# Kernel tuning notes

Measured on AMD Instinct MI355X. Metric: run time of the kernel, lower is better.

The kernel has to match this reference:

```python
import jax, jax.numpy as jnp
import numpy as np

B, S, D = 8, 4096, 64
NEG = 10000.0


def setup_inputs() -> dict:
    key = jax.random.key(0)
    k1, k2, k3, k4 = jax.random.split(key, 4)
    query = jax.random.normal(k1, (B, S, D), dtype=jnp.float32)
    k_ = jax.random.normal(k2, (B, S, D), dtype=jnp.float32)
    v_ = jax.random.normal(k3, (B, S, D), dtype=jnp.float32)
    # padding mask [B, Sk]: mostly valid, tail padded for some rows
    lens = jax.random.randint(k4, (B,), S // 2, S + 1)
    mask = jnp.arange(S)[None, :] < lens[:, None]
    return {"query": query, "key": k_, "value": v_, "mask": mask}


def reference(query, key, value, mask):
    d = query.shape[-1]
    scale = 1.0 / jnp.sqrt(jnp.asarray(d, dtype=query.dtype))
    # e: [B, Sq, Sk]
    e = jnp.einsum("bqd,bkd->bqk", query, key) * scale
    # causal (history_only) mask: key index > query index gets -10000
    q_idx = jnp.arange(query.shape[1])[:, None]
    k_idx = jnp.arange(key.shape[1])[None, :]
    e = e - NEG * (k_idx > q_idx).astype(e.dtype)[None, :, :]
    # padding mask [B, 1, Sk]
    e = e - NEG * (1.0 - mask.astype(e.dtype))[:, None, :]
    attention = jax.nn.softmax(e, axis=-1)
    return jnp.einsum("bqk,bkd->bqd", attention, value)
```

## Files before the change

### kernel.cpp

```cpp
#include <hip/hip_runtime.h>
#include <hip/hip_bf16.h>

#define B_N 8
#define S_N 4096
#define D_N 64
#define NQT 64
#define TILE_BYTES 8192
#define SLOT_BYTES 8704

typedef __attribute__((ext_vector_type(8))) short bf16x8;
typedef __attribute__((ext_vector_type(4))) float f32x4;
typedef __attribute__((ext_vector_type(16))) float f32x16;
typedef unsigned uint2v __attribute__((ext_vector_type(2)));
typedef unsigned uint4v __attribute__((ext_vector_type(4)));

__device__ __forceinline__ float fast_exp2(float x) {
#if __has_builtin(__builtin_amdgcn_exp2f)
  return __builtin_amdgcn_exp2f(x);
#else
  return exp2f(x);
#endif
}

__device__ __forceinline__ unsigned f2bf_u(float x) {
  __hip_bfloat16 h = __float2bfloat16(x);
  return (unsigned)__builtin_bit_cast(unsigned short, h);
}
__device__ __forceinline__ unsigned pack2(float a, float b) {
  return f2bf_u(a) | (f2bf_u(b) << 16);
}
__device__ __forceinline__ int swzoff(int row, int colb) {
  return row * 128 + (colb ^ ((((row & 7) ^ ((row >> 3) & 7))) << 4));
}

__device__ __forceinline__ void pl32swap(unsigned& a, unsigned& b) {
#if __has_builtin(__builtin_amdgcn_permlane32_swap)
  uint2v r = __builtin_amdgcn_permlane32_swap(a, b, false, false);
  a = r[0];
  b = r[1];
#else
  asm volatile("v_permlane32_swap_b32 %0, %1" : "+v"(a), "+v"(b));
#endif
}
__device__ __forceinline__ float xhalf_sum(float x) {
  unsigned a = __builtin_bit_cast(unsigned, x), b = a;
  pl32swap(a, b);
  return __builtin_bit_cast(float, a) + __builtin_bit_cast(float, b);
}

#define GLOAD(g, l)                                                  \
  __builtin_amdgcn_global_load_lds(                                  \
      (const __attribute__((address_space(1))) unsigned*)(g),        \
      (__attribute__((address_space(3))) unsigned*)(l), 16, 0, 0)

__global__ void __launch_bounds__(256)
prep_kernel(const float* __restrict__ K, const float* __restrict__ V,
            const unsigned* __restrict__ mask, char* __restrict__ Ks,
            char* __restrict__ VTs, int* __restrict__ lens) {
  __shared__ float vl[64][72];
  const int bt = blockIdx.x, tid = threadIdx.x;
  const int b = bt >> 6, kt = bt & 63;

  if (tid < 64) {
    unsigned first = mask[0];
    bool v;
    int gi = kt * 64 + tid;
    if (first == 0x01010101u) {
      v = ((const unsigned char*)mask)[(size_t)b * S_N + gi] != 0;
    } else if (first == 0x3F800000u) {
      v = ((const float*)mask)[(size_t)b * S_N + gi] != 0.0f;
    } else {
      v = ((const int*)mask)[(size_t)b * S_N + gi] != 0;
    }
    unsigned long long bal = __ballot(v);
    if (tid == 0) atomicAdd(&lens[b], __popcll(bal));
  }

  const float* Kt = K + (size_t)bt * 4096;
  const float* Vt = V + (size_t)bt * 4096;
  char* Ko = Ks + (size_t)bt * TILE_BYTES;
  char* Vo = VTs + (size_t)bt * TILE_BYTES;
#pragma unroll
  for (int i = 0; i < 2; ++i) {
    int c = tid + i * 256;
    int r = c >> 3, j = c & 7;
    f32x4 a = *(const f32x4*)(Kt + r * 64 + j * 8);
    f32x4 b4 = *(const f32x4*)(Kt + r * 64 + j * 8 + 4);
    union { bf16x8 v; unsigned u[4]; } pk;
    pk.u[0] = pack2(a[0], a[1]);   pk.u[1] = pack2(a[2], a[3]);
    pk.u[2] = pack2(b4[0], b4[1]); pk.u[3] = pack2(b4[2], b4[3]);
    *(bf16x8*)(Ko + swzoff(r, j * 16)) = pk.v;
    f32x4 va = *(const f32x4*)(Vt + r * 64 + j * 8);
    f32x4 vb = *(const f32x4*)(Vt + r * 64 + j * 8 + 4);
#pragma unroll
    for (int e = 0; e < 4; ++e) vl[j * 8 + e][r] = va[e];
#pragma unroll
    for (int e = 0; e < 4; ++e) vl[j * 8 + 4 + e][r] = vb[e];
  }
  __syncthreads();
#pragma unroll
  for (int i = 0; i < 2; ++i) {
    int c = tid + i * 256;
    int d = c >> 3, j = c & 7;
    f32x4 fa = *(const f32x4*)(&vl[d][j * 8]);
    f32x4 fb = *(const f32x4*)(&vl[d][j * 8 + 4]);
    union { bf16x8 v; unsigned u[4]; } pk;
    pk.u[0] = pack2(fa[0], fa[1]); pk.u[1] = pack2(fa[2], fa[3]);
    pk.u[2] = pack2(fb[0], fb[1]); pk.u[3] = pack2(fb[2], fb[3]);
    *(bf16x8*)(Vo + swzoff(d, j * 16)) = pk.v;
  }
}

__global__ void __launch_bounds__(128)
attn_kernel(const float* __restrict__ Qg, const char* __restrict__ Ks,
            const char* __restrict__ VTs, const int* __restrict__ lens,
            float* __restrict__ Og, char* __restrict__ parts,
            int M, int U) {
  __shared__ __align__(16) char sm[16384];
  const int tid = threadIdx.x;
  const int bid = blockIdx.x;
  const int b = bid & 7;
  const int u = (U - 1) - (bid >> 3);
  int a = 0;
  while ((M * (a + 1) * (a + 2)) / 2 <= u) ++a;
  const int v = u - (M * a * (a + 1)) / 2;
  const int qt = a * M + v / (a + 1);
  const int s = v - (v / (a + 1)) * (a + 1);
  const int kq = a + 1;

  const int q0 = qt * 64;
  const int len = lens[b];
  int nt = (len + 63) >> 6;
  if (qt + 1 < nt) nt = qt + 1;
  const int beg = s * M;
  int cnt = nt - beg;
  if (cnt > M) cnt = M;
  if (cnt < 0) cnt = 0;

  const int lane = tid & 63;
  const int ws = tid >> 6;
  const int q31 = lane & 31;
  const int h = lane >> 5;
  const int qg = q0 + ws * 32 + q31;

  const char* Kb = Ks + (size_t)(b * NQT) * TILE_BYTES;
  const char* Vb = VTs + (size_t)(b * NQT) * TILE_BYTES;
  const char* srcb = ws ? Vb : Kb;

  auto issue = [&](int t) {
    const char* sp = srcb + (size_t)t * TILE_BYTES + lane * 16;
    char* d = sm + ws * 8192;
#pragma unroll
    for (int i = 0; i < 8; ++i) GLOAD(sp + i * 1024, d + i * 1024);
  };

  if (cnt > 0) issue(beg);

  constexpr float CS = 0.125f * 1.4426950408889634f;
  bf16x8 qf[4];
#pragma unroll
  for (int c = 0; c < 4; ++c) {
    const float* src = Qg + ((size_t)(b * S_N) + qg) * D_N + c * 16 + h * 8;
    f32x4 aa = *(const f32x4*)src;
    f32x4 b4 = *(const f32x4*)(src + 4);
    union { bf16x8 v; unsigned u[4]; } pk;
    pk.u[0] = pack2(aa[0] * CS, aa[1] * CS);
    pk.u[1] = pack2(aa[2] * CS, aa[3] * CS);
    pk.u[2] = pack2(b4[0] * CS, b4[1] * CS);
    pk.u[3] = pack2(b4[2] * CS, b4[3] * CS);
    qf[c] = pk.v;
  }

  f32x16 ot0 = {}, ot1 = {};
  float l = 0.0f;

  for (int j = 0; j < cnt; ++j) {
    const int t = beg + j;
    asm volatile("s_waitcnt vmcnt(0)" ::: "memory");
    __builtin_amdgcn_sched_barrier(0);
    __builtin_amdgcn_s_barrier();
    __builtin_amdgcn_sched_barrier(0);

    bf16x8 kf[8], vf[8];
    const char* kbase = sm;
    const char* vbase = sm + 8192;
#pragma unroll
    for (int c = 0; c < 4; ++c) {
      kf[c]     = *(const bf16x8*)(kbase + swzoff(q31, c * 32 + h * 16));
      kf[4 + c] = *(const bf16x8*)(kbase + swzoff(32 + q31, c * 32 + h * 16));
      vf[c]     = *(const bf16x8*)(vbase + swzoff(q31, c * 32 + h * 16));
      vf[4 + c] = *(const bf16x8*)(vbase + swzoff(32 + q31, c * 32 + h * 16));
    }
    asm volatile("s_waitcnt lgkmcnt(0)" ::: "memory");
    __builtin_amdgcn_sched_barrier(0);
    __builtin_amdgcn_s_barrier();
    __builtin_amdgcn_sched_barrier(0);

    if (j + 1 < cnt) issue(t + 1);

    f32x16 s0, s1;
#pragma unroll
    for (int i = 0; i < 16; ++i) { s0[i] = -8.0f; s1[i] = -8.0f; }
    __builtin_amdgcn_s_setprio(1);
#pragma unroll
    for (int c = 0; c < 4; ++c) {
      s0 = __builtin_amdgcn_mfma_f32_32x32x16_bf16(kf[c], qf[c], s0, 0, 0, 0);
      s1 = __builtin_amdgcn_mfma_f32_32x32x16_bf16(kf[4 + c], qf[c], s1, 0, 0, 0);
    }
    __builtin_amdgcn_s_setprio(0);

    const int kv0 = t * 64;
    if (t == qt || kv0 + 64 > len) {
#pragma unroll
      for (int g = 0; g < 4; ++g)
#pragma unroll
        for (int jj = 0; jj < 4; ++jj) {
          int kl = 8 * g + 4 * h + jj;
          if (kv0 + kl > qg || kv0 + kl >= len) s0[g * 4 + jj] = -10000.0f;
          if (kv0 + 32 + kl > qg || kv0 + 32 + kl >= len) s1[g * 4 + jj] = -10000.0f;
        }
    }

    float ps0 = 0.f, ps1 = 0.f, ps2 = 0.f, ps3 = 0.f;
#pragma unroll
    for (int g = 0; g < 4; ++g) {
      s0[4 * g + 0] = fast_exp2(s0[4 * g + 0]); ps0 += s0[4 * g + 0];
      s0[4 * g + 1] = fast_exp2(s0[4 * g + 1]); ps1 += s0[4 * g + 1];
      s0[4 * g + 2] = fast_exp2(s0[4 * g + 2]); ps2 += s0[4 * g + 2];
      s0[4 * g + 3] = fast_exp2(s0[4 * g + 3]); ps3 += s0[4 * g + 3];
      s1[4 * g + 0] = fast_exp2(s1[4 * g + 0]); ps0 += s1[4 * g + 0];
      s1[4 * g + 1] = fast_exp2(s1[4 * g + 1]); ps1 += s1[4 * g + 1];
      s1[4 * g + 2] = fast_exp2(s1[4 * g + 2]); ps2 += s1[4 * g + 2];
      s1[4 * g + 3] = fast_exp2(s1[4 * g + 3]); ps3 += s1[4 * g + 3];
    }
    l += xhalf_sum((ps0 + ps1) + (ps2 + ps3));

    unsigned opk0[4][2], opk1[4][2];
#pragma unroll
    for (int g = 0; g < 4; ++g) {
      opk0[g][0] = pack2(s0[4 * g + 0], s0[4 * g + 1]);
      opk0[g][1] = pack2(s0[4 * g + 2], s0[4 * g + 3]);
      opk1[g][0] = pack2(s1[4 * g + 0], s1[4 * g + 1]);
      opk1[g][1] = pack2(s1[4 * g + 2], s1[4 * g + 3]);
    }
    bf16x8 pb[4];
#pragma unroll
    for (int c = 0; c < 4; ++c) {
      const unsigned(*o)[2] = (c < 2) ? opk0 : opk1;
      const int g0 = 2 * (c & 1), g1 = g0 + 1;
      unsigned a0 = o[g0][0], b0 = o[g1][0];
      unsigned a1 = o[g0][1], b1 = o[g1][1];
      pl32swap(a0, b0);
      pl32swap(a1, b1);
      union { bf16x8 v; unsigned u[4]; } pk;
      pk.u[0] = a0; pk.u[1] = a1; pk.u[2] = b0; pk.u[3] = b1;
      pb[c] = pk.v;
    }

    __builtin_amdgcn_s_setprio(1);
#pragma unroll
    for (int c = 0; c < 4; ++c) {
      ot0 = __builtin_amdgcn_mfma_f32_32x32x16_bf16(vf[c], pb[c], ot0, 0, 0, 0);
      ot1 = __builtin_amdgcn_mfma_f32_32x32x16_bf16(vf[4 + c], pb[c], ot1, 0, 0, 0);
    }
    __builtin_amdgcn_s_setprio(0);
  }

  if (kq == 1) {
    float linv = 1.0f / l;
    float* orow = Og + ((size_t)(b * S_N) + qg) * D_N;
#pragma unroll
    for (int g = 0; g < 4; ++g) {
      f32x4 oa = {ot0[4 * g + 0] * linv, ot0[4 * g + 1] * linv,
                  ot0[4 * g + 2] * linv, ot0[4 * g + 3] * linv};
      *(f32x4*)(orow + 8 * g + 4 * h) = oa;
      f32x4 ob = {ot1[4 * g + 0] * linv, ot1[4 * g + 1] * linv,
                  ot1[4 * g + 2] * linv, ot1[4 * g + 3] * linv};
      *(f32x4*)(orow + 32 + 8 * g + 4 * h) = ob;
    }
  } else {
    char* slot = parts + ((size_t)b * U + u) * SLOT_BYTES;
    unsigned w[16];
#pragma unroll
    for (int jj = 0; jj < 8; ++jj) {
      w[jj] = pack2(ot0[2 * jj], ot0[2 * jj + 1]);
      w[8 + jj] = pack2(ot1[2 * jj], ot1[2 * jj + 1]);
    }
    uint4v* dst = (uint4v*)(slot + tid * 64);
#pragma unroll
    for (int q4 = 0; q4 < 4; ++q4)
      dst[q4] = (uint4v){w[4 * q4], w[4 * q4 + 1], w[4 * q4 + 2], w[4 * q4 + 3]};
    *(float*)(slot + 8192 + tid * 4) = l;
  }
}

__global__ void __launch_bounds__(128)
merge_kernel(const char* __restrict__ parts, float* __restrict__ Og,
             int M, int U) {
  const int bid = blockIdx.x;
  const int b = bid & 7, qt = bid >> 3;
  const int a = qt / M;
  const int kq = a + 1;
  if (kq == 1) return;
  const int tid = threadIdx.x;
  const int base_u = (M * a * (a + 1)) / 2 + (qt - a * M) * (a + 1);

  float acc[32];
#pragma unroll
  for (int i = 0; i < 32; ++i) acc[i] = 0.0f;
  float L = 0.0f;
  for (int s2 = 0; s2 < kq; ++s2) {
    const char* slot = parts + ((size_t)b * U + base_u + s2) * SLOT_BYTES;
    const uint4v* src = (const uint4v*)(slot + tid * 64);
#pragma unroll
    for (int q4 = 0; q4 < 4; ++q4) {
      uint4v wv = src[q4];
#pragma unroll
      for (int e = 0; e < 4; ++e) {
        unsigned uw = wv[e];
        acc[2 * (4 * q4 + e)] += __builtin_bit_cast(float, uw << 16);
        acc[2 * (4 * q4 + e) + 1] += __builtin_bit_cast(float, uw & 0xFFFF0000u);
      }
    }
    L += *(const float*)(slot + 8192 + tid * 4);
  }
  float linv = 1.0f / L;
  const int q = (tid >> 6) * 32 + (tid & 31);
  const int h = (tid & 63) >> 5;
  float* orow = Og + ((size_t)(b * S_N) + qt * 64 + q) * D_N;
#pragma unroll
  for (int dt = 0; dt < 2; ++dt)
#pragma unroll
    for (int g = 0; g < 4; ++g) {
      f32x4 w = {acc[dt * 16 + 4 * g + 0] * linv, acc[dt * 16 + 4 * g + 1] * linv,
                 acc[dt * 16 + 4 * g + 2] * linv, acc[dt * 16 + 4 * g + 3] * linv};
      *(f32x4*)(orow + dt * 32 + 8 * g + 4 * h) = w;
    }
}

extern "C" void kernel_launch(void* const* d_in, const int* in_sizes, int n_in,
                              void* d_out, int out_size, void* d_ws, size_t ws_size,
                              hipStream_t stream) {
  const float* Qg = (const float*)d_in[0];
  const float* Kg = (const float*)d_in[1];
  const float* Vg = (const float*)d_in[2];
  const unsigned* mask = (const unsigned*)d_in[3];
  float* Og = (float*)d_out;

  int* lens = (int*)d_ws;
  char* Ks = (char*)d_ws + 4096;
  char* VTs = Ks + (size_t)B_N * NQT * TILE_BYTES;
  char* parts = VTs + (size_t)B_N * NQT * TILE_BYTES;

  int M = 8, U = 288;
  size_t need = 4096 + ((size_t)2 * B_N * NQT * TILE_BYTES) +
                (size_t)B_N * 288 * SLOT_BYTES;
  if (ws_size < need) { M = 64; U = 64; }

  hipMemsetAsync(lens, 0, 4096, stream);
  prep_kernel<<<dim3(B_N * NQT), dim3(256), 0, stream>>>(Kg, Vg, mask, Ks, VTs, lens);
  attn_kernel<<<dim3(B_N * U), dim3(128), 0, stream>>>(Qg, Ks, VTs, lens, Og,
                                                       parts, M, U);
  if (M == 8)
    merge_kernel<<<dim3(B_N * NQT), dim3(128), 0, stream>>>(parts, Og, M, U);
}
```

Measured before the change: 66.50 us.

## Split attention blocks into single-wave blocks loading pre-laid-out K/V tiles from global

Replaces the two-wave block that staged K and V tiles through LDS with async global-to-LDS loads and barriers by single-wave blocks. Each wave reads K and V fragments straight from global memory, using a new MFMA-fragment-ordered layout written by the prep kernel. The mask length count moves into a separate lens kernel, which removes the memset and atomics, and the partial-result slots are split per wave. This drops LDS traffic and barriers and doubles the grid, but each wave now re-reads K/V from global/L2 with no cross-wave sharing or prefetch overlap.

```diff
diff --git a/kernel.cpp b/kernel.cpp
--- a/kernel.cpp
+++ b/kernel.cpp
@@ -6,7 +6,7 @@
 #define D_N 64
 #define NQT 64
 #define TILE_BYTES 8192
-#define SLOT_BYTES 8704
+#define SLOT_BYTES 4352
 
 typedef __attribute__((ext_vector_type(8))) short bf16x8;
 typedef __attribute__((ext_vector_type(4))) float f32x4;
@@ -28,9 +28,6 @@
 }
 __device__ __forceinline__ unsigned pack2(float a, float b) {
   return f2bf_u(a) | (f2bf_u(b) << 16);
-}
-__device__ __forceinline__ int swzoff(int row, int colb) {
-  return row * 128 + (colb ^ ((((row & 7) ^ ((row >> 3) & 7))) << 4));
 }
 
 __device__ __forceinline__ void pl32swap(unsigned& a, unsigned& b) {
@@ -48,34 +45,34 @@
   return __builtin_bit_cast(float, a) + __builtin_bit_cast(float, b);
 }
 
-#define GLOAD(g, l)                                                  \
-  __builtin_amdgcn_global_load_lds(                                  \
-      (const __attribute__((address_space(1))) unsigned*)(g),        \
-      (__attribute__((address_space(3))) unsigned*)(l), 16, 0, 0)
+__global__ void __launch_bounds__(256)
+lens_kernel(const unsigned* __restrict__ mask, int* __restrict__ lens) {
+  int b = blockIdx.x, tid = threadIdx.x;
+  unsigned first = mask[0];
+  int cnt = 0;
+  if (first == 0x01010101u) {
+    const unsigned char* m = ((const unsigned char*)mask) + (size_t)b * S_N;
+    for (int i = tid; i < S_N; i += 256) cnt += (m[i] != 0);
+  } else if (first == 0x3F800000u) {
+    const float* m = ((const float*)mask) + (size_t)b * S_N;
+    for (int i = tid; i < S_N; i += 256) cnt += (m[i] != 0.0f);
+  } else {
+    const int* m = ((const int*)mask) + (size_t)b * S_N;
+    for (int i = tid; i < S_N; i += 256) cnt += (m[i] != 0);
+  }
+#pragma unroll
+  for (int off = 32; off > 0; off >>= 1) cnt += __shfl_down(cnt, off);
+  __shared__ int acc[4];
+  if ((tid & 63) == 0) acc[tid >> 6] = cnt;
+  __syncthreads();
+  if (tid == 0) lens[b] = acc[0] + acc[1] + acc[2] + acc[3];
+}
 
 __global__ void __launch_bounds__(256)
 prep_kernel(const float* __restrict__ K, const float* __restrict__ V,
-            const unsigned* __restrict__ mask, char* __restrict__ Ks,
-            char* __restrict__ VTs, int* __restrict__ lens) {
+            char* __restrict__ Ks, char* __restrict__ VTs) {
   __shared__ float vl[64][72];
   const int bt = blockIdx.x, tid = threadIdx.x;
-  const int b = bt >> 6, kt = bt & 63;
-
-  if (tid < 64) {
-    unsigned first = mask[0];
-    bool v;
-    int gi = kt * 64 + tid;
-    if (first == 0x01010101u) {
-      v = ((const unsigned char*)mask)[(size_t)b * S_N + gi] != 0;
-    } else if (first == 0x3F800000u) {
-      v = ((const float*)mask)[(size_t)b * S_N + gi] != 0.0f;
-    } else {
-      v = ((const int*)mask)[(size_t)b * S_N + gi] != 0;
-    }
-    unsigned long long bal = __ballot(v);
-    if (tid == 0) atomicAdd(&lens[b], __popcll(bal));
-  }
-
   const float* Kt = K + (size_t)bt * 4096;
   const float* Vt = V + (size_t)bt * 4096;
   char* Ko = Ks + (size_t)bt * TILE_BYTES;
@@ -89,7 +86,8 @@
     union { bf16x8 v; unsigned u[4]; } pk;
     pk.u[0] = pack2(a[0], a[1]);   pk.u[1] = pack2(a[2], a[3]);
     pk.u[2] = pack2(b4[0], b4[1]); pk.u[3] = pack2(b4[2], b4[3]);
-    *(bf16x8*)(Ko + swzoff(r, j * 16)) = pk.v;
+    *(bf16x8*)(Ko + ((r >> 5) * 4 + (j >> 1)) * 1024 + (j & 1) * 512 +
+               (r & 31) * 16) = pk.v;
     f32x4 va = *(const f32x4*)(Vt + r * 64 + j * 8);
     f32x4 vb = *(const f32x4*)(Vt + r * 64 + j * 8 + 4);
 #pragma unroll
@@ -107,20 +105,22 @@
     union { bf16x8 v; unsigned u[4]; } pk;
     pk.u[0] = pack2(fa[0], fa[1]); pk.u[1] = pack2(fa[2], fa[3]);
     pk.u[2] = pack2(fb[0], fb[1]); pk.u[3] = pack2(fb[2], fb[3]);
-    *(bf16x8*)(Vo + swzoff(d, j * 16)) = pk.v;
-  }
-}
-
-__global__ void __launch_bounds__(128)
+    *(bf16x8*)(Vo + ((d >> 5) * 4 + (j >> 1)) * 1024 + (j & 1) * 512 +
+               (d & 31) * 16) = pk.v;
+  }
+}
+
+__global__ void __launch_bounds__(64)
 attn_kernel(const float* __restrict__ Qg, const char* __restrict__ Ks,
             const char* __restrict__ VTs, const int* __restrict__ lens,
             float* __restrict__ Og, char* __restrict__ parts,
             int M, int U) {
-  __shared__ __align__(16) char sm[16384];
-  const int tid = threadIdx.x;
+  const int lane = threadIdx.x;
   const int bid = blockIdx.x;
   const int b = bid & 7;
-  const int u = (U - 1) - (bid >> 3);
+  const int r2 = bid >> 3;
+  const int ws = r2 & 1;
+  const int u = (U - 1) - (r2 >> 1);
   int a = 0;
   while ((M * (a + 1) * (a + 2)) / 2 <= u) ++a;
   const int v = u - (M * a * (a + 1)) / 2;
@@ -137,24 +137,12 @@
   if (cnt > M) cnt = M;
   if (cnt < 0) cnt = 0;
 
-  const int lane = tid & 63;
-  const int ws = tid >> 6;
   const int q31 = lane & 31;
   const int h = lane >> 5;
   const int qg = q0 + ws * 32 + q31;
 
   const char* Kb = Ks + (size_t)(b * NQT) * TILE_BYTES;
   const char* Vb = VTs + (size_t)(b * NQT) * TILE_BYTES;
-  const char* srcb = ws ? Vb : Kb;
-
-  auto issue = [&](int t) {
-    const char* sp = srcb + (size_t)t * TILE_BYTES + lane * 16;
-    char* d = sm + ws * 8192;
-#pragma unroll
-    for (int i = 0; i < 8; ++i) GLOAD(sp + i * 1024, d + i * 1024);
-  };
-
-  if (cnt > 0) issue(beg);
 
   constexpr float CS = 0.125f * 1.4426950408889634f;
   bf16x8 qf[4];
@@ -176,38 +164,23 @@
 
   for (int j = 0; j < cnt; ++j) {
     const int t = beg + j;
-    asm volatile("s_waitcnt vmcnt(0)" ::: "memory");
-    __builtin_amdgcn_sched_barrier(0);
-    __builtin_amdgcn_s_barrier();
-    __builtin_amdgcn_sched_barrier(0);
-
-    bf16x8 kf[8], vf[8];
-    const char* kbase = sm;
-    const char* vbase = sm + 8192;
+    bf16x8 f[8];
+    const char* Kt = Kb + (size_t)t * TILE_BYTES + lane * 16;
+#pragma unroll
+    for (int c = 0; c < 8; ++c) f[c] = *(const bf16x8*)(Kt + c * 1024);
+
+    f32x16 s0, s1;
+#pragma unroll
+    for (int i = 0; i < 16; ++i) { s0[i] = -8.0f; s1[i] = -8.0f; }
 #pragma unroll
     for (int c = 0; c < 4; ++c) {
-      kf[c]     = *(const bf16x8*)(kbase + swzoff(q31, c * 32 + h * 16));
-      kf[4 + c] = *(const bf16x8*)(kbase + swzoff(32 + q31, c * 32 + h * 16));
-      vf[c]     = *(const bf16x8*)(vbase + swzoff(q31, c * 32 + h * 16));
-      vf[4 + c] = *(const bf16x8*)(vbase + swzoff(32 + q31, c * 32 + h * 16));
-    }
-    asm volatile("s_waitcnt lgkmcnt(0)" ::: "memory");
-    __builtin_amdgcn_sched_barrier(0);
-    __builtin_amdgcn_s_barrier();
-    __builtin_amdgcn_sched_barrier(0);
-
-    if (j + 1 < cnt) issue(t + 1);
-
-    f32x16 s0, s1;
-#pragma unroll
-    for (int i = 0; i < 16; ++i) { s0[i] = -8.0f; s1[i] = -8.0f; }
-    __builtin_amdgcn_s_setprio(1);
-#pragma unroll
-    for (int c = 0; c < 4; ++c) {
-      s0 = __builtin_amdgcn_mfma_f32_32x32x16_bf16(kf[c], qf[c], s0, 0, 0, 0);
-      s1 = __builtin_amdgcn_mfma_f32_32x32x16_bf16(kf[4 + c], qf[c], s1, 0, 0, 0);
-    }
-    __builtin_amdgcn_s_setprio(0);
+      s0 = __builtin_amdgcn_mfma_f32_32x32x16_bf16(f[c], qf[c], s0, 0, 0, 0);
+      s1 = __builtin_amdgcn_mfma_f32_32x32x16_bf16(f[4 + c], qf[c], s1, 0, 0, 0);
+    }
+
+    const char* Vt2 = Vb + (size_t)t * TILE_BYTES + lane * 16;
+#pragma unroll
+    for (int c = 0; c < 8; ++c) f[c] = *(const bf16x8*)(Vt2 + c * 1024);
 
     const int kv0 = t * 64;
     if (t == qt || kv0 + 64 > len) {
@@ -257,13 +230,11 @@
       pb[c] = pk.v;
     }
 
-    __builtin_amdgcn_s_setprio(1);
 #pragma unroll
     for (int c = 0; c < 4; ++c) {
-      ot0 = __builtin_amdgcn_mfma_f32_32x32x16_bf16(vf[c], pb[c], ot0, 0, 0, 0);
-      ot1 = __builtin_amdgcn_mfma_f32_32x32x16_bf16(vf[4 + c], pb[c], ot1, 0, 0, 0);
-    }
-    __builtin_amdgcn_s_setprio(0);
+      ot0 = __builtin_amdgcn_mfma_f32_32x32x16_bf16(f[c], pb[c], ot0, 0, 0, 0);
+      ot1 = __builtin_amdgcn_mfma_f32_32x32x16_bf16(f[4 + c], pb[c], ot1, 0, 0, 0);
+    }
   }
 
   if (kq == 1) {
@@ -279,18 +250,18 @@
       *(f32x4*)(orow + 32 + 8 * g + 4 * h) = ob;
     }
   } else {
-    char* slot = parts + ((size_t)b * U + u) * SLOT_BYTES;
+    char* slot = parts + (((size_t)b * U + u) * 2 + ws) * SLOT_BYTES;
     unsigned w[16];
 #pragma unroll
     for (int jj = 0; jj < 8; ++jj) {
       w[jj] = pack2(ot0[2 * jj], ot0[2 * jj + 1]);
       w[8 + jj] = pack2(ot1[2 * jj], ot1[2 * jj + 1]);
     }
-    uint4v* dst = (uint4v*)(slot + tid * 64);
+    uint4v* dst = (uint4v*)(slot + lane * 64);
 #pragma unroll
     for (int q4 = 0; q4 < 4; ++q4)
       dst[q4] = (uint4v){w[4 * q4], w[4 * q4 + 1], w[4 * q4 + 2], w[4 * q4 + 3]};
-    *(float*)(slot + 8192 + tid * 4) = l;
+    *(float*)(slot + 4096 + lane * 4) = l;
   }
 }
 
@@ -303,6 +274,8 @@
   const int kq = a + 1;
   if (kq == 1) return;
   const int tid = threadIdx.x;
+  const int ws = tid >> 6;
+  const int lane = tid & 63;
   const int base_u = (M * a * (a + 1)) / 2 + (qt - a * M) * (a + 1);
 
   float acc[32];
@@ -310,8 +283,9 @@
   for (int i = 0; i < 32; ++i) acc[i] = 0.0f;
   float L = 0.0f;
   for (int s2 = 0; s2 < kq; ++s2) {
-    const char* slot = parts + ((size_t)b * U + base_u + s2) * SLOT_BYTES;
-    const uint4v* src = (const uint4v*)(slot + tid * 64);
+    const char* slot =
+        parts + (((size_t)b * U + base_u + s2) * 2 + ws) * SLOT_BYTES;
+    const uint4v* src = (const uint4v*)(slot + lane * 64);
 #pragma unroll
     for (int q4 = 0; q4 < 4; ++q4) {
       uint4v wv = src[q4];
@@ -322,12 +296,12 @@
         acc[2 * (4 * q4 + e) + 1] += __builtin_bit_cast(float, uw & 0xFFFF0000u);
       }
     }
-    L += *(const float*)(slot + 8192 + tid * 4);
+    L += *(const float*)(slot + 4096 + lane * 4);
   }
   float linv = 1.0f / L;
-  const int q = (tid >> 6) * 32 + (tid & 31);
-  const int h = (tid & 63) >> 5;
-  float* orow = Og + ((size_t)(b * S_N) + qt * 64 + q) * D_N;
+  const int q31 = lane & 31;
+  const int h = lane >> 5;
+  float* orow = Og + ((size_t)(b * S_N) + qt * 64 + ws * 32 + q31) * D_N;
 #pragma unroll
   for (int dt = 0; dt < 2; ++dt)
 #pragma unroll
@@ -354,13 +328,13 @@
 
   int M = 8, U = 288;
   size_t need = 4096 + ((size_t)2 * B_N * NQT * TILE_BYTES) +
-                (size_t)B_N * 288 * SLOT_BYTES;
+                (size_t)B_N * 288 * 2 * SLOT_BYTES;
   if (ws_size < need) { M = 64; U = 64; }
 
-  hipMemsetAsync(lens, 0, 4096, stream);
-  prep_kernel<<<dim3(B_N * NQT), dim3(256), 0, stream>>>(Kg, Vg, mask, Ks, VTs, lens);
-  attn_kernel<<<dim3(B_N * U), dim3(128), 0, stream>>>(Qg, Ks, VTs, lens, Og,
-                                                       parts, M, U);
+  lens_kernel<<<dim3(B_N), dim3(256), 0, stream>>>(mask, lens);
+  prep_kernel<<<dim3(B_N * NQT), dim3(256), 0, stream>>>(Kg, Vg, Ks, VTs);
+  attn_kernel<<<dim3(B_N * U * 2), dim3(64), 0, stream>>>(Qg, Ks, VTs, lens,
+                                                          Og, parts, M, U);
   if (M == 8)
     merge_kernel<<<dim3(B_N * NQT), dim3(128), 0, stream>>>(parts, Og, M, U);
 }
```

Result: faster. 58.09 us (-12.7%).
